# Performance work log

Measured on AMD Instinct MI355X. Metric: run time of the kernel, lower is better.

The kernel has to match this reference:

```python
import jax, jax.numpy as jnp
import numpy as np

B, T, D, K = 8, 2048, 768, 2048

def setup_inputs() -> dict:
    key = jax.random.key(0)
    k1, k2 = jax.random.split(key)
    token = jax.random.normal(k1, (B, T, D), dtype=jnp.float32)
    codebook = jax.random.normal(k2, (K, D), dtype=jnp.float32)
    return {"token": token, "codebook": codebook}

def reference(token, codebook):
    x_sq = jnp.sum(token * token, axis=-1, keepdims=True)          # [B,T,1]
    e_sq = jnp.sum(codebook * codebook, axis=-1)                   # [K]
    dots = jnp.einsum('btd,kd->btk', token, codebook)              # [B,T,K]
    dist = x_sq - 2.0 * dots + e_sq                                # [B,T,K]
    indices = jnp.argmin(dist, axis=-1)                            # [B,T] int
    quantize = codebook[indices]                                   # [B,T,D] gather
    # commitment loss: mse(sg(quantize), x)
    commit_loss = jnp.mean(jnp.square(jax.lax.stop_gradient(quantize) - token))
    # straight-through estimator
    quantized = token + jax.lax.stop_gradient(quantize - token)
    return quantized, indices, commit_loss
```

## Files before the change

kernel.cpp:

```cpp
#include <hip/hip_runtime.h>

#define M_TOK 16384
#define D_DIM 768
#define K_CB  2048

#define BTOK  64
#define BCODE 512
#define BK    32
#define KSPLIT 4
#define NT    (D_DIM / BK)
#define NSLOT 16
#define EPS   0.25f

typedef __attribute__((ext_vector_type(8))) short bf16x8;
typedef __attribute__((ext_vector_type(4))) float f32x4;

__device__ __forceinline__ unsigned short f2bf(float x) {
    unsigned u = __float_as_uint(x);
    return (unsigned short)((u + 0x7fffu + ((u >> 16) & 1u)) >> 16);
}
__device__ __forceinline__ float bf2f(unsigned short h) {
    return __uint_as_float((unsigned)h << 16);
}

#define ASYNC16(gp, lp) __builtin_amdgcn_global_load_lds( \
    (const __attribute__((address_space(1))) void*)(gp),  \
    (__attribute__((address_space(3))) void*)(lp), 16, 0, 0)

__global__ void vq_prep(const float* __restrict__ cb,
                        const float* __restrict__ tok,
                        unsigned short* __restrict__ cb_hi,
                        unsigned short* __restrict__ cb_lo,
                        float* __restrict__ esq,
                        unsigned short* __restrict__ tok_hi,
                        unsigned short* __restrict__ tok_lo) {
    const int bid = blockIdx.x;
    if (bid < 512) {
        const int w = threadIdx.x >> 6, lane = threadIdx.x & 63;
        const int k = bid * 4 + w;
        const float* row = cb + (size_t)k * D_DIM;
        unsigned short* hk = cb_hi + (size_t)k * D_DIM;
        unsigned short* lk = cb_lo + (size_t)k * D_DIM;
        float s = 0.f;
        for (int j = lane; j < D_DIM; j += 64) {
            float x = row[j];
            s = fmaf(x, x, s);
            unsigned short h = f2bf(x);
            hk[j] = h;
            lk[j] = f2bf(x - bf2f(h));
        }
        #pragma unroll
        for (int off = 32; off; off >>= 1) s += __shfl_down(s, off);
        if (!lane) esq[k] = s;
    } else {
        const int N8 = (M_TOK * D_DIM) / 8;
        const int stride = 256 * 256;
        for (int i = (bid - 512) * 256 + threadIdx.x; i < N8; i += stride) {
            const float4 a = *(const float4*)(tok + (size_t)i * 8);
            const float4 b = *(const float4*)(tok + (size_t)i * 8 + 4);
            const float v[8] = {a.x, a.y, a.z, a.w, b.x, b.y, b.z, b.w};
            unsigned hh[8], ll[8];
            #pragma unroll
            for (int j = 0; j < 8; ++j) {
                const unsigned short h = f2bf(v[j]);
                hh[j] = h;
                ll[j] = f2bf(v[j] - bf2f(h));
            }
            uint4 ph, pl;
            ph.x = hh[0] | (hh[1] << 16);  ph.y = hh[2] | (hh[3] << 16);
            ph.z = hh[4] | (hh[5] << 16);  ph.w = hh[6] | (hh[7] << 16);
            pl.x = ll[0] | (ll[1] << 16);  pl.y = ll[2] | (ll[3] << 16);
            pl.z = ll[4] | (ll[5] << 16);  pl.w = ll[6] | (ll[7] << 16);
            *(uint4*)(tok_hi + (size_t)i * 8) = ph;
            *(uint4*)(tok_lo + (size_t)i * 8) = pl;
        }
    }
}

__launch_bounds__(512, 4)
__global__ void vq_dist(const unsigned short* __restrict__ tok_hi,
                        const unsigned short* __restrict__ tok_lo,
                        const unsigned short* __restrict__ cb_hi,
                        const unsigned short* __restrict__ cb_lo,
                        const float* __restrict__ esq,
                        float4* __restrict__ top2) {
    __shared__ unsigned short sAh[BCODE * BK];
    __shared__ unsigned short sAl[BCODE * BK];
    __shared__ unsigned short sBh[BTOK * BK];
    __shared__ unsigned short sBl[BTOK * BK];
    __shared__ float sE[BCODE];

    const int tid  = threadIdx.x;
    const int lane = tid & 63;
    const int w    = tid >> 6;

    const int bid = blockIdx.x;
    const int xcd = bid & 7;
    const int m   = bid >> 3;
    const int ksl = xcd >> 1;
    const int txi = m | ((xcd & 1) << 7);
    const int tokBase = txi * BTOK;
    const int kBase   = ksl * BCODE;

    for (int j = tid; j < BCODE; j += 512) sE[j] = esq[kBase + j];

    int gOffA[4], ldsA[4];
    #pragma unroll
    for (int q = 0; q < 4; ++q) {
        const int G   = q * 512 + tid;
        const int row = G >> 2;
        const int sl  = (G & 3) ^ ((row >> 1) & 3);
        gOffA[q] = row * D_DIM + sl * 8;
        ldsA[q]  = G * 16;
    }
    const int gB   = tid & 255;
    const int rowB = gB >> 2;
    const int slB  = (gB & 3) ^ ((rowB >> 1) & 3);
    const int gOffB = rowB * D_DIM + slB * 8;
    const int ldsB  = gB * 16;

    const unsigned short* pAh = cb_hi + (size_t)kBase * D_DIM;
    const unsigned short* pAl = cb_lo + (size_t)kBase * D_DIM;
    const unsigned short* pBsel = ((tid < 256) ? tok_hi : tok_lo)
                                  + (size_t)tokBase * D_DIM;
    char* sBsel = (tid < 256) ? (char*)sBh : (char*)sBl;

    const int h  = lane >> 4;
    const int lm = lane & 15;
    const int wr = w >> 1;
    const int wc = wr * 128;
    const int wt = (w & 1) * 32;
    int offA[8], offB[2];
    #pragma unroll
    for (int i = 0; i < 8; ++i) {
        const int rA = wc + i * 16 + lm;
        offA[i] = rA * 64 + ((h ^ ((rA >> 1) & 3)) * 16);
    }
    #pragma unroll
    for (int j = 0; j < 2; ++j) {
        const int rB = wt + j * 16 + lm;
        offB[j] = rB * 64 + ((h ^ ((rB >> 1) & 3)) * 16);
    }

    f32x4 acc[8][2];
    #pragma unroll
    for (int i = 0; i < 8; ++i)
        #pragma unroll
        for (int j = 0; j < 2; ++j) acc[i][j] = (f32x4){0.f, 0.f, 0.f, 0.f};

    for (int t = 0; t < NT; ++t) {
        const int dco = t * BK;
        __syncthreads();
        #pragma unroll
        for (int q = 0; q < 4; ++q) {
            ASYNC16(pAh + gOffA[q] + dco, (char*)sAh + ldsA[q]);
            ASYNC16(pAl + gOffA[q] + dco, (char*)sAl + ldsA[q]);
        }
        ASYNC16(pBsel + gOffB + dco, sBsel + ldsB);
        __syncthreads();

        bf16x8 bh[2], bl[2];
        #pragma unroll
        for (int j = 0; j < 2; ++j) {
            bh[j] = *(const bf16x8*)((const char*)sBh + offB[j]);
            bl[j] = *(const bf16x8*)((const char*)sBl + offB[j]);
        }
        #pragma unroll
        for (int i = 0; i < 8; ++i) {
            const bf16x8 ah = *(const bf16x8*)((const char*)sAh + offA[i]);
            acc[i][0] = __builtin_amdgcn_mfma_f32_16x16x32_bf16(ah, bh[0], acc[i][0], 0, 0, 0);
            acc[i][1] = __builtin_amdgcn_mfma_f32_16x16x32_bf16(ah, bh[1], acc[i][1], 0, 0, 0);
            acc[i][0] = __builtin_amdgcn_mfma_f32_16x16x32_bf16(ah, bl[0], acc[i][0], 0, 0, 0);
            acc[i][1] = __builtin_amdgcn_mfma_f32_16x16x32_bf16(ah, bl[1], acc[i][1], 0, 0, 0);
            const bf16x8 al = *(const bf16x8*)((const char*)sAl + offA[i]);
            acc[i][0] = __builtin_amdgcn_mfma_f32_16x16x32_bf16(al, bh[0], acc[i][0], 0, 0, 0);
            acc[i][1] = __builtin_amdgcn_mfma_f32_16x16x32_bf16(al, bh[1], acc[i][1], 0, 0, 0);
        }
    }

    #pragma unroll
    for (int j = 0; j < 2; ++j) {
        float m1 = 3.4e38f, m2 = 3.4e38f;
        int   k1 = 0x7fffffff, k2 = 0x7fffffff;
        #pragma unroll
        for (int i = 0; i < 8; ++i)
            #pragma unroll
            for (int r = 0; r < 4; ++r) {
                const int cl = wc + i * 16 + (lane >> 4) * 4 + r;
                const float s = sE[cl] - 2.0f * acc[i][j][r];
                const int kg = kBase + cl;
                if (s < m1)      { m2 = m1; k2 = k1; m1 = s; k1 = kg; }
                else if (s < m2) { m2 = s; k2 = kg; }
            }
        #pragma unroll
        for (int off = 16; off <= 32; off <<= 1) {
            const float om1 = __shfl_xor(m1, off); const int ok1 = __shfl_xor(k1, off);
            const float om2 = __shfl_xor(m2, off); const int ok2 = __shfl_xor(k2, off);
            const bool aB = (m1 < om1) || (m1 == om1 && k1 < ok1);
            float n1m, n2m; int n1k, n2k;
            if (aB) {
                n1m = m1; n1k = k1;
                const bool c = (om1 < m2) || (om1 == m2 && ok1 < k2);
                n2m = c ? om1 : m2; n2k = c ? ok1 : k2;
            } else {
                n1m = om1; n1k = ok1;
                const bool c = (m1 < om2) || (m1 == om2 && k1 < ok2);
                n2m = c ? m1 : om2; n2k = c ? k1 : ok2;
            }
            m1 = n1m; k1 = n1k; m2 = n2m; k2 = n2k;
        }
        if (lane < 16) {
            const int tt = tokBase + wt + j * 16 + lane;
            top2[(size_t)tt * NSLOT + (ksl * 4 + wr)] =
                make_float4(m1, __int_as_float(k1), m2, __int_as_float(k2));
        }
    }
}

__global__ void vq_final(const float* __restrict__ token,
                         const float* __restrict__ cb,
                         const float* __restrict__ esq,
                         const float4* __restrict__ top2,
                         float* __restrict__ out_q,
                         float* __restrict__ out_idx,
                         float* __restrict__ out_loss) {
    const int w = threadIdx.x >> 6, lane = threadIdx.x & 63;
    const int t = blockIdx.x * 4 + w;

    const float4 sv = top2[(size_t)t * NSLOT + (lane & 15)];
    float m1 = sv.x, m2 = sv.z;
    int   k1 = __float_as_int(sv.y), k2 = __float_as_int(sv.w);
    #pragma unroll
    for (int off = 1; off <= 8; off <<= 1) {
        const float om1 = __shfl_xor(m1, off); const int ok1 = __shfl_xor(k1, off);
        const float om2 = __shfl_xor(m2, off); const int ok2 = __shfl_xor(k2, off);
        const bool aB = (m1 < om1) || (m1 == om1 && k1 < ok1);
        float n1m, n2m; int n1k, n2k;
        if (aB) {
            n1m = m1; n1k = k1;
            const bool c = (om1 < m2) || (om1 == m2 && ok1 < k2);
            n2m = c ? om1 : m2; n2k = c ? ok1 : k2;
        } else {
            n1m = om1; n1k = ok1;
            const bool c = (m1 < om2) || (m1 == om2 && k1 < ok2);
            n2m = c ? m1 : om2; n2k = c ? k1 : ok2;
        }
        m1 = n1m; k1 = n1k; m2 = n2m; k2 = n2k;
    }

    unsigned choice = (unsigned)k1;
    if (!(m2 - m1 > EPS)) {
        const float* tr = token + (size_t)t * D_DIM;
        const float* c1 = cb + (size_t)k1 * D_DIM;
        const float* c2 = cb + (size_t)k2 * D_DIM;
        float d1 = 0.f, d2 = 0.f;
        for (int e = lane; e < D_DIM; e += 64) {
            const float x = tr[e];
            d1 = fmaf(c1[e], x, d1);
            d2 = fmaf(c2[e], x, d2);
        }
        #pragma unroll
        for (int off = 32; off; off >>= 1) {
            d1 += __shfl_down(d1, off);
            d2 += __shfl_down(d2, off);
        }
        d1 = __shfl(d1, 0);
        d2 = __shfl(d2, 0);
        const float s1 = esq[k1] - 2.f * d1;
        const float s2 = esq[k2] - 2.f * d2;
        if (s2 < s1 || (s2 == s1 && k2 < k1)) choice = (unsigned)k2;
    }

    const float* crow = cb + (size_t)choice * D_DIM;
    const float* trow = token + (size_t)t * D_DIM;
    float*       qrow = out_q + (size_t)t * D_DIM;
    float lsum = 0.f;
    #pragma unroll
    for (int u = 0; u < 3; ++u) {
        const int e = (u * 64 + lane) * 4;
        const float4 q = *(const float4*)(crow + e);
        const float4 x = *(const float4*)(trow + e);
        *(float4*)(qrow + e) = q;
        const float dx = q.x - x.x, dy = q.y - x.y, dz = q.z - x.z, dw = q.w - x.w;
        lsum += dx * dx + dy * dy + dz * dz + dw * dw;
    }
    if (!lane) out_idx[t] = (float)choice;

    #pragma unroll
    for (int off = 32; off; off >>= 1) lsum += __shfl_down(lsum, off);
    __shared__ float ws4[4];
    if (!lane) ws4[w] = lsum;
    __syncthreads();
    if (!threadIdx.x)
        atomicAdd(out_loss, (ws4[0] + ws4[1] + ws4[2] + ws4[3]) *
                            (1.0f / (float)((size_t)M_TOK * D_DIM)));
}

extern "C" void kernel_launch(void* const* d_in, const int* in_sizes, int n_in,
                              void* d_out, int out_size, void* d_ws, size_t ws_size,
                              hipStream_t stream) {
    const float* token = (const float*)d_in[0];
    const float* cb    = (const float*)d_in[1];

    float* out_q    = (float*)d_out;
    float* out_idx  = out_q + (size_t)M_TOK * D_DIM;
    float* out_loss = out_idx + M_TOK;

    unsigned short* tok_hi = (unsigned short*)out_q;
    unsigned short* tok_lo = tok_hi + (size_t)M_TOK * D_DIM;

    char* ws = (char*)d_ws;
    unsigned short* cb_hi = (unsigned short*)(ws);
    unsigned short* cb_lo = (unsigned short*)(ws + 3145728);
    float*          esq   = (float*)(ws + 6291456);
    float4*         top2  = (float4*)(ws + 6299648);

    hipMemsetAsync(out_loss, 0, sizeof(float), stream);

    vq_prep<<<768, 256, 0, stream>>>(cb, token, cb_hi, cb_lo, esq,
                                     tok_hi, tok_lo);

    vq_dist<<<(M_TOK / BTOK) * KSPLIT, 512, 0, stream>>>(
        tok_hi, tok_lo, cb_hi, cb_lo, esq, top2);

    vq_final<<<M_TOK / 4, 256, 0, stream>>>(token, cb, esq, top2,
                                            out_q, out_idx, out_loss);
}
```

Measured before the change: 331.3 us.

## Retile distance GEMM to square tiles with double-buffered LDS and in-block top2 merge

Reshapes the vq_dist tile from 512 codes x 64 tokens to 256x256 with 8 code splits. Each wave now holds a 4x8 accumulator block, which raises operand reuse per LDS load. It double-buffers the LDS stages so the global-to-LDS loads for the next K-slice overlap with the MFMA work, merges the per-wave top-2 candidates inside the block through shared scratch, and halves the slots the final kernel must reduce. It also folds the loss memset into the prep kernel. The cost is more LDS and more registers, with occupancy lowered to 2 blocks per CU, and only 512 blocks in the grid, which may underfill the GPU.

```diff
diff --git a/kernel.cpp b/kernel.cpp
--- a/kernel.cpp
+++ b/kernel.cpp
@@ -4,12 +4,12 @@
 #define D_DIM 768
 #define K_CB  2048
 
-#define BTOK  64
-#define BCODE 512
+#define BTOK  256
+#define BCODE 256
 #define BK    32
-#define KSPLIT 4
+#define KSPLIT 8
 #define NT    (D_DIM / BK)
-#define NSLOT 16
+#define NSLOT 8
 #define EPS   0.25f
 
 typedef __attribute__((ext_vector_type(8))) short bf16x8;
@@ -33,9 +33,11 @@
                         unsigned short* __restrict__ cb_lo,
                         float* __restrict__ esq,
                         unsigned short* __restrict__ tok_hi,
-                        unsigned short* __restrict__ tok_lo) {
+                        unsigned short* __restrict__ tok_lo,
+                        float* __restrict__ out_loss) {
     const int bid = blockIdx.x;
     if (bid < 512) {
+        if (bid == 511 && threadIdx.x == 0) *out_loss = 0.f;
         const int w = threadIdx.x >> 6, lane = threadIdx.x & 63;
         const int k = bid * 4 + w;
         const float* row = cb + (size_t)k * D_DIM;
@@ -77,118 +79,128 @@
     }
 }
 
-__launch_bounds__(512, 4)
+__launch_bounds__(512, 2)
 __global__ void vq_dist(const unsigned short* __restrict__ tok_hi,
                         const unsigned short* __restrict__ tok_lo,
                         const unsigned short* __restrict__ cb_hi,
                         const unsigned short* __restrict__ cb_lo,
                         const float* __restrict__ esq,
                         float4* __restrict__ top2) {
-    __shared__ unsigned short sAh[BCODE * BK];
-    __shared__ unsigned short sAl[BCODE * BK];
-    __shared__ unsigned short sBh[BTOK * BK];
-    __shared__ unsigned short sBl[BTOK * BK];
-    __shared__ float sE[BCODE];
+    __shared__ __align__(16) unsigned short sAh[2][BCODE * BK];
+    __shared__ __align__(16) unsigned short sAl[2][BCODE * BK];
+    __shared__ __align__(16) unsigned short sBh[2][BTOK * BK];
+    __shared__ __align__(16) unsigned short sBl[2][BTOK * BK];
 
     const int tid  = threadIdx.x;
     const int lane = tid & 63;
     const int w    = tid >> 6;
 
     const int bid = blockIdx.x;
-    const int xcd = bid & 7;
-    const int m   = bid >> 3;
-    const int ksl = xcd >> 1;
-    const int txi = m | ((xcd & 1) << 7);
+    const int ksl = bid & 7;
+    const int txi = bid >> 3;
     const int tokBase = txi * BTOK;
     const int kBase   = ksl * BCODE;
 
-    for (int j = tid; j < BCODE; j += 512) sE[j] = esq[kBase + j];
-
-    int gOffA[4], ldsA[4];
-    #pragma unroll
-    for (int q = 0; q < 4; ++q) {
+    int gOff[2], gLds[2];
+    #pragma unroll
+    for (int q = 0; q < 2; ++q) {
         const int G   = q * 512 + tid;
         const int row = G >> 2;
         const int sl  = (G & 3) ^ ((row >> 1) & 3);
-        gOffA[q] = row * D_DIM + sl * 8;
-        ldsA[q]  = G * 16;
-    }
-    const int gB   = tid & 255;
-    const int rowB = gB >> 2;
-    const int slB  = (gB & 3) ^ ((rowB >> 1) & 3);
-    const int gOffB = rowB * D_DIM + slB * 8;
-    const int ldsB  = gB * 16;
+        gOff[q] = row * D_DIM + sl * 8;
+        gLds[q] = G * 16;
+    }
 
     const unsigned short* pAh = cb_hi + (size_t)kBase * D_DIM;
     const unsigned short* pAl = cb_lo + (size_t)kBase * D_DIM;
-    const unsigned short* pBsel = ((tid < 256) ? tok_hi : tok_lo)
-                                  + (size_t)tokBase * D_DIM;
-    char* sBsel = (tid < 256) ? (char*)sBh : (char*)sBl;
+    const unsigned short* pBh = tok_hi + (size_t)tokBase * D_DIM;
+    const unsigned short* pBl = tok_lo + (size_t)tokBase * D_DIM;
 
     const int h  = lane >> 4;
     const int lm = lane & 15;
-    const int wr = w >> 1;
-    const int wc = wr * 128;
-    const int wt = (w & 1) * 32;
-    int offA[8], offB[2];
-    #pragma unroll
-    for (int i = 0; i < 8; ++i) {
+    const int wr = w & 3;
+    const int wc = wr * 64;
+    const int wt = w >> 2;
+    const int wtb = wt * 128;
+    int offA[4], offB[8];
+    #pragma unroll
+    for (int i = 0; i < 4; ++i) {
         const int rA = wc + i * 16 + lm;
         offA[i] = rA * 64 + ((h ^ ((rA >> 1) & 3)) * 16);
     }
     #pragma unroll
-    for (int j = 0; j < 2; ++j) {
-        const int rB = wt + j * 16 + lm;
+    for (int j = 0; j < 8; ++j) {
+        const int rB = wtb + j * 16 + lm;
         offB[j] = rB * 64 + ((h ^ ((rB >> 1) & 3)) * 16);
     }
 
-    f32x4 acc[8][2];
-    #pragma unroll
-    for (int i = 0; i < 8; ++i)
-        #pragma unroll
-        for (int j = 0; j < 2; ++j) acc[i][j] = (f32x4){0.f, 0.f, 0.f, 0.f};
-
-    for (int t = 0; t < NT; ++t) {
-        const int dco = t * BK;
+    f32x4 acc[4][8];
+    #pragma unroll
+    for (int i = 0; i < 4; ++i)
+        #pragma unroll
+        for (int j = 0; j < 8; ++j) acc[i][j] = (f32x4){0.f, 0.f, 0.f, 0.f};
+
+#define STAGE(b, t) do {                                                    \
+        const int dco = (t) * BK;                                           \
+        _Pragma("unroll")                                                   \
+        for (int q = 0; q < 2; ++q) {                                       \
+            ASYNC16(pAh + gOff[q] + dco, (char*)&sAh[b][0] + gLds[q]);      \
+            ASYNC16(pAl + gOff[q] + dco, (char*)&sAl[b][0] + gLds[q]);      \
+            ASYNC16(pBh + gOff[q] + dco, (char*)&sBh[b][0] + gLds[q]);      \
+            ASYNC16(pBl + gOff[q] + dco, (char*)&sBl[b][0] + gLds[q]);      \
+        }                                                                   \
+    } while (0)
+
+#define COMPUTE(b) do {                                                     \
+        bf16x8 ah[4], al[4];                                                \
+        _Pragma("unroll")                                                   \
+        for (int i = 0; i < 4; ++i) {                                       \
+            ah[i] = *(const bf16x8*)((const char*)&sAh[b][0] + offA[i]);    \
+            al[i] = *(const bf16x8*)((const char*)&sAl[b][0] + offA[i]);    \
+        }                                                                   \
+        _Pragma("unroll")                                                   \
+        for (int j = 0; j < 8; ++j) {                                       \
+            const bf16x8 bh = *(const bf16x8*)((const char*)&sBh[b][0] + offB[j]); \
+            const bf16x8 bl = *(const bf16x8*)((const char*)&sBl[b][0] + offB[j]); \
+            _Pragma("unroll")                                               \
+            for (int i = 0; i < 4; ++i) {                                   \
+                acc[i][j] = __builtin_amdgcn_mfma_f32_16x16x32_bf16(ah[i], bh, acc[i][j], 0, 0, 0); \
+                acc[i][j] = __builtin_amdgcn_mfma_f32_16x16x32_bf16(ah[i], bl, acc[i][j], 0, 0, 0); \
+                acc[i][j] = __builtin_amdgcn_mfma_f32_16x16x32_bf16(al[i], bh, acc[i][j], 0, 0, 0); \
+            }                                                               \
+        }                                                                   \
+    } while (0)
+
+    STAGE(0, 0);
+    __syncthreads();
+    for (int t = 0; t < NT - 1; ++t) {
+        STAGE((t + 1) & 1, t + 1);
+        COMPUTE(t & 1);
         __syncthreads();
-        #pragma unroll
-        for (int q = 0; q < 4; ++q) {
-            ASYNC16(pAh + gOffA[q] + dco, (char*)sAh + ldsA[q]);
-            ASYNC16(pAl + gOffA[q] + dco, (char*)sAl + ldsA[q]);
-        }
-        ASYNC16(pBsel + gOffB + dco, sBsel + ldsB);
-        __syncthreads();
-
-        bf16x8 bh[2], bl[2];
-        #pragma unroll
-        for (int j = 0; j < 2; ++j) {
-            bh[j] = *(const bf16x8*)((const char*)sBh + offB[j]);
-            bl[j] = *(const bf16x8*)((const char*)sBl + offB[j]);
-        }
-        #pragma unroll
-        for (int i = 0; i < 8; ++i) {
-            const bf16x8 ah = *(const bf16x8*)((const char*)sAh + offA[i]);
-            acc[i][0] = __builtin_amdgcn_mfma_f32_16x16x32_bf16(ah, bh[0], acc[i][0], 0, 0, 0);
-            acc[i][1] = __builtin_amdgcn_mfma_f32_16x16x32_bf16(ah, bh[1], acc[i][1], 0, 0, 0);
-            acc[i][0] = __builtin_amdgcn_mfma_f32_16x16x32_bf16(ah, bl[0], acc[i][0], 0, 0, 0);
-            acc[i][1] = __builtin_amdgcn_mfma_f32_16x16x32_bf16(ah, bl[1], acc[i][1], 0, 0, 0);
-            const bf16x8 al = *(const bf16x8*)((const char*)sAl + offA[i]);
-            acc[i][0] = __builtin_amdgcn_mfma_f32_16x16x32_bf16(al, bh[0], acc[i][0], 0, 0, 0);
-            acc[i][1] = __builtin_amdgcn_mfma_f32_16x16x32_bf16(al, bh[1], acc[i][1], 0, 0, 0);
-        }
-    }
-
-    #pragma unroll
-    for (int j = 0; j < 2; ++j) {
+    }
+    COMPUTE((NT - 1) & 1);
+
+#undef STAGE
+#undef COMPUTE
+
+    float es[4][4];
+    #pragma unroll
+    for (int i = 0; i < 4; ++i)
+        #pragma unroll
+        for (int r = 0; r < 4; ++r)
+            es[i][r] = esq[kBase + wc + i * 16 + (lane >> 4) * 4 + r];
+
+    float4* scr = (float4*)&sAh[0][0];
+    #pragma unroll
+    for (int j = 0; j < 8; ++j) {
         float m1 = 3.4e38f, m2 = 3.4e38f;
         int   k1 = 0x7fffffff, k2 = 0x7fffffff;
         #pragma unroll
-        for (int i = 0; i < 8; ++i)
+        for (int i = 0; i < 4; ++i)
             #pragma unroll
             for (int r = 0; r < 4; ++r) {
-                const int cl = wc + i * 16 + (lane >> 4) * 4 + r;
-                const float s = sE[cl] - 2.0f * acc[i][j][r];
-                const int kg = kBase + cl;
+                const float s = es[i][r] - 2.0f * acc[i][j][r];
+                const int kg = kBase + wc + i * 16 + (lane >> 4) * 4 + r;
                 if (s < m1)      { m2 = m1; k2 = k1; m1 = s; k1 = kg; }
                 else if (s < m2) { m2 = s; k2 = kg; }
             }
@@ -209,11 +221,36 @@
             }
             m1 = n1m; k1 = n1k; m2 = n2m; k2 = n2k;
         }
-        if (lane < 16) {
-            const int tt = tokBase + wt + j * 16 + lane;
-            top2[(size_t)tt * NSLOT + (ksl * 4 + wr)] =
+        if (lane < 16)
+            scr[(wtb + j * 16 + lane) * 4 + wr] =
                 make_float4(m1, __int_as_float(k1), m2, __int_as_float(k2));
-        }
+    }
+    __syncthreads();
+
+    if (tid < BTOK) {
+        const float4 c0 = scr[tid * 4 + 0];
+        float m1 = c0.x, m2 = c0.z;
+        int   k1 = __float_as_int(c0.y), k2 = __float_as_int(c0.w);
+        #pragma unroll
+        for (int s = 1; s < 4; ++s) {
+            const float4 sv = scr[tid * 4 + s];
+            const float om1 = sv.x, om2 = sv.z;
+            const int ok1 = __float_as_int(sv.y), ok2 = __float_as_int(sv.w);
+            const bool aB = (m1 < om1) || (m1 == om1 && k1 < ok1);
+            float n1m, n2m; int n1k, n2k;
+            if (aB) {
+                n1m = m1; n1k = k1;
+                const bool c = (om1 < m2) || (om1 == m2 && ok1 < k2);
+                n2m = c ? om1 : m2; n2k = c ? ok1 : k2;
+            } else {
+                n1m = om1; n1k = ok1;
+                const bool c = (m1 < om2) || (m1 == om2 && k1 < ok2);
+                n2m = c ? m1 : om2; n2k = c ? k1 : ok2;
+            }
+            m1 = n1m; k1 = n1k; m2 = n2m; k2 = n2k;
+        }
+        top2[(size_t)(tokBase + tid) * NSLOT + ksl] =
+            make_float4(m1, __int_as_float(k1), m2, __int_as_float(k2));
     }
 }
 
@@ -227,11 +264,11 @@
     const int w = threadIdx.x >> 6, lane = threadIdx.x & 63;
     const int t = blockIdx.x * 4 + w;
 
-    const float4 sv = top2[(size_t)t * NSLOT + (lane & 15)];
+    const float4 sv = top2[(size_t)t * NSLOT + (lane & 7)];
     float m1 = sv.x, m2 = sv.z;
     int   k1 = __float_as_int(sv.y), k2 = __float_as_int(sv.w);
     #pragma unroll
-    for (int off = 1; off <= 8; off <<= 1) {
+    for (int off = 1; off <= 4; off <<= 1) {
         const float om1 = __shfl_xor(m1, off); const int ok1 = __shfl_xor(k1, off);
         const float om2 = __shfl_xor(m2, off); const int ok2 = __shfl_xor(k2, off);
         const bool aB = (m1 < om1) || (m1 == om1 && k1 < ok1);
@@ -315,10 +352,8 @@
     float*          esq   = (float*)(ws + 6291456);
     float4*         top2  = (float4*)(ws + 6299648);
 
-    hipMemsetAsync(out_loss, 0, sizeof(float), stream);
-
     vq_prep<<<768, 256, 0, stream>>>(cb, token, cb_hi, cb_lo, esq,
-                                     tok_hi, tok_lo);
+                                     tok_hi, tok_lo, out_loss);
 
     vq_dist<<<(M_TOK / BTOK) * KSPLIT, 512, 0, stream>>>(
         tok_hi, tok_lo, cb_hi, cb_lo, esq, top2);
```

After: 315.9 us. 4.7% less time.
